# Kernel optimization log

Measured on AMD Instinct MI355X. Metric: run time of the kernel, lower is better.

Reference implementation:

```python
import jax, jax.numpy as jnp
import numpy as np

HIDDEN = 1024
HEADS = 16
HEAD_DIM = HIDDEN // HEADS


def setup_inputs() -> dict:
    key = jax.random.key(0)
    ks = jax.random.split(key, 5)
    B, T = 4, 2048
    x = jax.random.normal(ks[0], (B, T, HIDDEN), dtype=jnp.float32)
    s = 1.0 / np.sqrt(HIDDEN)
    qkv_w = jax.random.normal(ks[1], (HIDDEN, 3 * HIDDEN), dtype=jnp.float32) * s
    qkv_b = jnp.zeros((3 * HIDDEN,), dtype=jnp.float32)
    proj_w = jax.random.normal(ks[2], (HIDDEN, HIDDEN), dtype=jnp.float32) * s
    proj_b = jnp.zeros((HIDDEN,), dtype=jnp.float32)
    return {"x": x, "qkv_w": qkv_w, "qkv_b": qkv_b, "proj_w": proj_w, "proj_b": proj_b}


def reference(x, qkv_w, qkv_b, proj_w, proj_b):
    B, T, C = x.shape
    qkv = x @ qkv_w + qkv_b                       # [B,T,3C]
    qkv = qkv.reshape(B, T, 3, HEADS, HEAD_DIM)
    q, k, v = qkv[:, :, 0], qkv[:, :, 1], qkv[:, :, 2]  # [B,T,H,D]
    scale = HEAD_DIM ** -0.5
    scores = jnp.einsum('bthd,bshd->bhts', q, k) * scale  # [B,H,T,T]
    attn = jax.nn.softmax(scores, axis=-1)
    out = jnp.einsum('bhts,bshd->bthd', attn, v).reshape(B, T, C)
    return out @ proj_w + proj_b
```

## Files before the change

kernel.cpp:

```cpp
#include <hip/hip_runtime.h>
#include <hip/hip_bf16.h>

#define HID  1024
#define N3   3072
#define NH   16
#define HD   64
#define SEQ  2048
#define NB   4
#define MTOT 8192

typedef unsigned short u16x8 __attribute__((ext_vector_type(8)));
typedef unsigned short u16x4 __attribute__((ext_vector_type(4)));
typedef float f32x4 __attribute__((ext_vector_type(4)));

static __device__ __forceinline__ unsigned short f2bf(float f) {
    union { float f; unsigned u; } v; v.f = f;
    unsigned r = (v.u + 0x7fffu + ((v.u >> 16) & 1u)) >> 16;
    return (unsigned short)r;
}

static __device__ __forceinline__ float fexp2(float x) {
    float r; asm("v_exp_f32 %0, %1" : "=v"(r) : "v"(x)); return r;
}

typedef __attribute__((address_space(3))) void* lds_vp;
typedef const __attribute__((address_space(1))) void* gbl_vp;

static __device__ __forceinline__ void gload16(const void* g, void* l) {
    __builtin_amdgcn_global_load_lds((gbl_vp)g, (lds_vp)l, 16, 0, 0);
}

#define CQ 0.18033688011112042f

__device__ __forceinline__ void tcvt_tile(const float* __restrict__ W,
                                          unsigned short* __restrict__ WT,
                                          int R, int C, int tile, int tid,
                                          unsigned short* tilebuf) {
    int tiles_c = C >> 6;
    int k0 = (tile / tiles_c) << 6;
    int n0 = (tile % tiles_c) << 6;
    #pragma unroll
    for (int it = 0; it < 2; ++it) {
        int task = it * 256 + tid;
        int t = task >> 3, dc = task & 7;
        const float* src = W + (size_t)(k0 + t) * C + n0 + dc * 8;
        float4 a = *(const float4*)src;
        float4 b = *(const float4*)(src + 4);
        u16x8 p;
        p[0]=f2bf(a.x); p[1]=f2bf(a.y); p[2]=f2bf(a.z); p[3]=f2bf(a.w);
        p[4]=f2bf(b.x); p[5]=f2bf(b.y); p[6]=f2bf(b.z); p[7]=f2bf(b.w);
        *(u16x8*)&tilebuf[t * 64 + ((dc ^ (t & 7)) << 3)] = p;
    }
    __syncthreads();
    #pragma unroll
    for (int it = 0; it < 2; ++it) {
        int task = it * 256 + tid;
        int d = task >> 3, tc = task & 7;
        u16x8 p;
        #pragma unroll
        for (int i = 0; i < 8; ++i) {
            int ii = (i + tc) & 7;
            int t = tc * 8 + ii;
            p[ii] = tilebuf[t * 64 + ((((d >> 3) ^ (t & 7)) << 3)) + (d & 7)];
        }
        *(u16x8*)(WT + (size_t)(n0 + d) * R + k0 + tc * 8) = p;
    }
}

__global__ __launch_bounds__(256) void k_prep(const float* __restrict__ x,
                                              unsigned short* __restrict__ xb,
                                              const float* __restrict__ qkv_w,
                                              unsigned short* __restrict__ wqkvT,
                                              const float* __restrict__ proj_w,
                                              unsigned short* __restrict__ wprojT) {
    __shared__ unsigned short tilebuf[64 * 64];
    int blk = blockIdx.x, tid = threadIdx.x;
    if (blk < 4096) {
        int i = (blk * 256 + tid) * 8;
        float4 a = *(const float4*)(x + i);
        float4 b = *(const float4*)(x + i + 4);
        u16x8 p;
        p[0]=f2bf(a.x); p[1]=f2bf(a.y); p[2]=f2bf(a.z); p[3]=f2bf(a.w);
        p[4]=f2bf(b.x); p[5]=f2bf(b.y); p[6]=f2bf(b.z); p[7]=f2bf(b.w);
        *(u16x8*)(xb + i) = p;
    } else if (blk < 4864) {
        tcvt_tile(qkv_w, wqkvT, HID, N3, blk - 4096, tid, tilebuf);
    } else {
        tcvt_tile(proj_w, wprojT, HID, HID, blk - 4864, tid, tilebuf);
    }
}

template<int MODE>
__global__ __launch_bounds__(256) void k_gemm(const unsigned short* __restrict__ A,
                                              const unsigned short* __restrict__ BT,
                                              const float* __restrict__ bias,
                                              void* __restrict__ C1, void* __restrict__ C2,
                                              int M, int N, int K) {
    int tiles_n = N >> 7;
    int bid = (blockIdx.x & 7) * (gridDim.x >> 3) + (blockIdx.x >> 3);
    int bm = bid / tiles_n, bn = bid % tiles_n;
    int tid = threadIdx.x, wid = tid >> 6, lane = tid & 63;
    int wr = wid >> 1, wc = wid & 1;
    int fr = lane & 15, fg = lane >> 4;

    __shared__ unsigned short lA[128 * 64];
    __shared__ unsigned short lB[128 * 64];

    f32x4 acc[4][4];
    #pragma unroll
    for (int m = 0; m < 4; ++m)
        #pragma unroll
        for (int n = 0; n < 4; ++n)
            acc[m][n] = (f32x4){0.f, 0.f, 0.f, 0.f};

    int srow = lane >> 3;
    int sch  = (lane & 7) ^ srow;
    const unsigned short* aSrc[4]; const unsigned short* bSrc[4];
    unsigned short* aDst[4]; unsigned short* bDst[4];
    #pragma unroll
    for (int i = 0; i < 4; ++i) {
        int rbase = i * 32 + wid * 8;
        aSrc[i] = A  + (size_t)(bm * 128 + rbase + srow) * K + sch * 8;
        bSrc[i] = BT + (size_t)(bn * 128 + rbase + srow) * K + sch * 8;
        aDst[i] = lA + rbase * 64;
        bDst[i] = lB + rbase * 64;
    }

    for (int k0 = 0; k0 < K; k0 += 64) {
        __syncthreads();
        #pragma unroll
        for (int i = 0; i < 4; ++i) {
            gload16(aSrc[i] + k0, aDst[i]);
            gload16(bSrc[i] + k0, bDst[i]);
        }
        asm volatile("s_waitcnt vmcnt(0)" ::: "memory");
        __syncthreads();
        #pragma unroll
        for (int kk = 0; kk < 2; ++kk) {
            u16x8 af[4], bf[4];
            #pragma unroll
            for (int m = 0; m < 4; ++m) {
                int row = wr * 64 + m * 16 + fr;
                int ch = ((kk << 2) + fg) ^ (fr & 7);
                af[m] = *(const u16x8*)&lA[row * 64 + ch * 8];
            }
            #pragma unroll
            for (int n = 0; n < 4; ++n) {
                int row = wc * 64 + n * 16 + fr;
                int ch = ((kk << 2) + fg) ^ (fr & 7);
                bf[n] = *(const u16x8*)&lB[row * 64 + ch * 8];
            }
            #pragma unroll
            for (int m = 0; m < 4; ++m)
                #pragma unroll
                for (int n = 0; n < 4; ++n)
                    acc[m][n] = __builtin_amdgcn_mfma_f32_16x16x32_bf16(af[m], bf[n], acc[m][n], 0, 0, 0);
        }
    }

    if (MODE == 0) {
        float* C = (float*)C1;
        #pragma unroll
        for (int n = 0; n < 4; ++n) {
            int col = bn * 128 + wc * 64 + n * 16 + fr;
            float bv = bias[col];
            #pragma unroll
            for (int m = 0; m < 4; ++m) {
                int row0 = bm * 128 + wr * 64 + m * 16 + fg * 4;
                #pragma unroll
                for (int r = 0; r < 4; ++r)
                    C[(size_t)(row0 + r) * N + col] = acc[m][n][r] + bv;
            }
        }
    } else {
        if (bn < 16) {
            unsigned short* qkb = (unsigned short*)C1;
            #pragma unroll
            for (int n = 0; n < 4; ++n) {
                int col = bn * 128 + wc * 64 + n * 16 + fr;
                float bv = bias[col];
                float cs = (col < 1024) ? CQ : 1.0f;
                #pragma unroll
                for (int m = 0; m < 4; ++m) {
                    int row0 = bm * 128 + wr * 64 + m * 16 + fg * 4;
                    #pragma unroll
                    for (int r = 0; r < 4; ++r)
                        qkb[(size_t)(row0 + r) * 2048 + col] = f2bf((acc[m][n][r] + bv) * cs);
                }
            }
        } else {
            unsigned short* vT = (unsigned short*)C2;
            #pragma unroll
            for (int n = 0; n < 4; ++n) {
                int col = bn * 128 + wc * 64 + n * 16 + fr;
                float bv = bias[col];
                int cv = col - 2048;
                int hh = cv >> 6, d = cv & 63;
                #pragma unroll
                for (int m = 0; m < 4; ++m) {
                    int row0 = bm * 128 + wr * 64 + m * 16 + fg * 4;
                    int bb = row0 >> 11, t0 = row0 & 2047;
                    u16x4 st;
                    #pragma unroll
                    for (int r = 0; r < 4; ++r) st[r] = f2bf(acc[m][n][r] + bv);
                    *(u16x4*)&vT[((size_t)((bb * 16 + hh) * 64 + d)) * 2048 + t0] = st;
                }
            }
        }
    }
}

__global__ __launch_bounds__(256) void k_attn(const unsigned short* __restrict__ qkb,
                                              const unsigned short* __restrict__ vT,
                                              unsigned short* __restrict__ out) {
    int bid = (blockIdx.x & 7) * 128 + (blockIdx.x >> 3);
    int bh = bid >> 4;
    int q0 = (bid & 15) << 7;
    int b = bh >> 4, h = bh & 15;
    int tid = threadIdx.x, wid = tid >> 6, lane = tid & 63;
    int fr = lane & 15, fg = lane >> 4;

    __shared__ unsigned short lK[2][8192];
    __shared__ unsigned short lV[2][8192];
    const char* lKb = (const char*)lK;
    const char* lVb = (const char*)lV;

    int srow = lane >> 3;
    int sch  = (lane & 7) ^ srow;
    int woff = wid * 512;

    u16x8 ones;
    #pragma unroll
    for (int i = 0; i < 8; ++i) ones[i] = 0x3F80;

    int kfb[2], vbb[4];
    #pragma unroll
    for (int kk = 0; kk < 2; ++kk) kfb[kk] = fr * 128 + (((((kk << 2) + fg) ^ (fr & 7))) << 4);
    #pragma unroll
    for (int kk = 0; kk < 4; ++kk) vbb[kk] = fr * 256 + (((((kk << 2) + fg) ^ (fr & 7))) << 4);

    const unsigned short* qbase = qkb + (size_t)(b * SEQ) * 2048 + h * 64;
    #pragma unroll
    for (int i = 0; i < 4; ++i) {
        int rbase = i * 32 + wid * 8;
        gload16(qbase + (size_t)(q0 + rbase + srow) * 2048 + sch * 8, (unsigned short*)lK + rbase * 64);
    }
    asm volatile("s_waitcnt vmcnt(0)" ::: "memory");
    __syncthreads();
    u16x8 qf[2][2];
    #pragma unroll
    for (int j = 0; j < 2; ++j)
        #pragma unroll
        for (int kk = 0; kk < 2; ++kk)
            qf[j][kk] = *(const u16x8*)(lKb + kfb[kk] + (wid * 32 + j * 16) * 128);
    __syncthreads();

    f32x4 o[2][4];
    #pragma unroll
    for (int j = 0; j < 2; ++j)
        #pragma unroll
        for (int i = 0; i < 4; ++i)
            o[j][i] = (f32x4){0.f, 0.f, 0.f, 0.f};
    f32x4 o_sum[2];
    o_sum[0] = (f32x4){0.f, 0.f, 0.f, 0.f};
    o_sum[1] = (f32x4){0.f, 0.f, 0.f, 0.f};

    const unsigned short* kp[4]; const unsigned short* vp[4];
    {
        const unsigned short* kbase = qkb + (size_t)(b * SEQ) * 2048 + 1024 + h * 64;
        const unsigned short* vbase = vT + (size_t)(bh * 64) * SEQ;
        #pragma unroll
        for (int i = 0; i < 4; ++i) {
            kp[i] = kbase + (size_t)(i * 32 + wid * 8 + srow) * 2048 + sch * 8;
            int vrow = i * 16 + wid * 4 + (lane >> 4);
            int vch = (lane & 15) ^ (vrow & 7);
            vp[i] = vbase + (size_t)vrow * SEQ + vch * 8;
        }
    }

#define STAGE(bufi) do {                                                   \
        unsigned short* kd = (unsigned short*)lK + (bufi) * 8192 + woff;   \
        unsigned short* vd = (unsigned short*)lV + (bufi) * 8192 + woff;   \
        _Pragma("unroll")                                                  \
        for (int i = 0; i < 4; ++i) {                                      \
            gload16(kp[i], kd + i * 2048);  kp[i] += 128 * 2048;           \
            gload16(vp[i], vd + i * 2048);  vp[i] += 128;                  \
        }                                                                  \
    } while (0)

    STAGE(0);

    for (int t = 0; t < 16; ++t) {
        int cur = t & 1;
        int cb = cur * 16384;
        if (t < 15) {
            STAGE(cur ^ 1);
            asm volatile("s_waitcnt vmcnt(8)" ::: "memory");
        } else {
            asm volatile("s_waitcnt vmcnt(0)" ::: "memory");
        }
        __builtin_amdgcn_s_barrier();
        __builtin_amdgcn_sched_barrier(0);

        u16x8 pb[2][4];
        #pragma unroll
        for (int ih = 0; ih < 2; ++ih) {
            f32x4 sa[2][4];
            #pragma unroll
            for (int j = 0; j < 2; ++j)
                #pragma unroll
                for (int il = 0; il < 4; ++il)
                    sa[j][il] = (f32x4){0.f, 0.f, 0.f, 0.f};
            #pragma unroll
            for (int kk = 0; kk < 2; ++kk) {
                u16x8 kf[4];
                #pragma unroll
                for (int il = 0; il < 4; ++il)
                    kf[il] = *(const u16x8*)(lKb + cb + kfb[kk] + (ih * 4 + il) * 2048);
                #pragma unroll
                for (int j = 0; j < 2; ++j)
                    #pragma unroll
                    for (int il = 0; il < 4; ++il)
                        sa[j][il] = __builtin_amdgcn_mfma_f32_16x16x32_bf16(kf[il], qf[j][kk], sa[j][il], 0, 0, 0);
            }

            #pragma unroll
            for (int j = 0; j < 2; ++j) {
                unsigned pk[2][2][2];
                #pragma unroll
                for (int il = 0; il < 4; ++il) {
                    #pragma unroll
                    for (int p = 0; p < 2; ++p) {
                        float ea = fexp2(sa[j][il][2 * p]);
                        float eb = fexp2(sa[j][il][2 * p + 1]);
                        unsigned rr;
                        asm("v_cvt_pk_bf16_f32 %0, %1, %2" : "=v"(rr) : "v"(ea), "v"(eb));
                        pk[il >> 1][il & 1][p] = rr;
                    }
                }
                #pragma unroll
                for (int t2 = 0; t2 < 2; ++t2) {
                    #pragma unroll
                    for (int p = 0; p < 2; ++p) {
                        asm("v_permlane32_swap_b32 %0, %1" : "+v"(pk[t2][0][p]), "+v"(pk[t2][1][p]));
                        asm("v_permlane16_swap_b32 %0, %1" : "+v"(pk[t2][0][p]), "+v"(pk[t2][1][p]));
                    }
                    union { unsigned u[4]; u16x8 v; } w;
                    w.u[0] = pk[t2][0][0]; w.u[1] = pk[t2][0][1];
                    w.u[2] = pk[t2][1][0]; w.u[3] = pk[t2][1][1];
                    pb[j][ih * 2 + t2] = w.v;
                    o_sum[j] = __builtin_amdgcn_mfma_f32_16x16x32_bf16(ones, pb[j][ih * 2 + t2], o_sum[j], 0, 0, 0);
                }
            }
        }

        #pragma unroll
        for (int kk = 0; kk < 4; ++kk) {
            u16x8 vb[4];
            #pragma unroll
            for (int i = 0; i < 4; ++i)
                vb[i] = *(const u16x8*)(lVb + cb + vbb[kk] + i * 4096);
            #pragma unroll
            for (int j = 0; j < 2; ++j)
                #pragma unroll
                for (int i = 0; i < 4; ++i)
                    o[j][i] = __builtin_amdgcn_mfma_f32_16x16x32_bf16(vb[i], pb[j][kk], o[j][i], 0, 0, 0);
        }

        __syncthreads();
    }
#undef STAGE

    #pragma unroll
    for (int j = 0; j < 2; ++j) {
        float inv = 1.f / o_sum[j][0];
        size_t t = q0 + wid * 32 + j * 16 + fr;
        #pragma unroll
        for (int i = 0; i < 4; ++i) {
            u16x4 st;
            st[0] = f2bf(o[j][i][0] * inv);
            st[1] = f2bf(o[j][i][1] * inv);
            st[2] = f2bf(o[j][i][2] * inv);
            st[3] = f2bf(o[j][i][3] * inv);
            *(u16x4*)&out[(size_t)(b * SEQ + t) * HID + h * 64 + i * 16 + fg * 4] = st;
        }
    }
}

extern "C" void kernel_launch(void* const* d_in, const int* in_sizes, int n_in,
                              void* d_out, int out_size, void* d_ws, size_t ws_size,
                              hipStream_t stream) {
    const float* x      = (const float*)d_in[0];
    const float* qkv_w  = (const float*)d_in[1];
    const float* qkv_b  = (const float*)d_in[2];
    const float* proj_w = (const float*)d_in[3];
    const float* proj_b = (const float*)d_in[4];
    float* out = (float*)d_out;

    char* ws = (char*)d_ws;
    unsigned short* xb     = (unsigned short*)ws;
    unsigned short* wqkvT  = (unsigned short*)(ws + 16777216);
    unsigned short* wprojT = (unsigned short*)(ws + 23068672);
    unsigned short* qkb    = (unsigned short*)(ws + 25165824);
    unsigned short* vTb    = (unsigned short*)(ws + 58720256);
    unsigned short* aob    = (unsigned short*)(ws + 75497472);

    k_prep<<<5120, 256, 0, stream>>>(x, xb, qkv_w, wqkvT, proj_w, wprojT);
    k_gemm<1><<<1536, 256, 0, stream>>>(xb, wqkvT, qkv_b, (void*)qkb, (void*)vTb, MTOT, N3, HID);
    k_attn<<<1024, 256, 0, stream>>>(qkb, vTb, aob);
    k_gemm<0><<<512, 256, 0, stream>>>(aob, wprojT, proj_b, (void*)out, nullptr, MTOT, HID, HID);
}
```

Before: 199.3 us.

## Double-buffer GEMM LDS stages and enlarge tiles to 256x128 with 512 threads

The GEMM kernel now uses 512-thread blocks computing 256x128 output tiles, with two dynamic-LDS buffers so the global-to-LDS load of the next K tile overlaps MFMA work on the current one. Grids are halved to match the larger tiles. This targets global-load latency stalls and the per-tile barrier cost, and raises reuse of each B tile. In exchange, each block needs 96KB of LDS, which limits occupancy, and the launch now also makes host-side attribute calls.

```diff
diff --git a/kernel.cpp b/kernel.cpp
--- a/kernel.cpp
+++ b/kernel.cpp
@@ -91,20 +91,20 @@
 }
 
 template<int MODE>
-__global__ __launch_bounds__(256) void k_gemm(const unsigned short* __restrict__ A,
-                                              const unsigned short* __restrict__ BT,
-                                              const float* __restrict__ bias,
-                                              void* __restrict__ C1, void* __restrict__ C2,
-                                              int M, int N, int K) {
+__global__ __launch_bounds__(512, 2) void k_gemm(const unsigned short* __restrict__ A,
+                                                 const unsigned short* __restrict__ BT,
+                                                 const float* __restrict__ bias,
+                                                 void* __restrict__ C1, void* __restrict__ C2,
+                                                 int M, int N, int K) {
+    extern __shared__ char ls[];
     int tiles_n = N >> 7;
     int bid = (blockIdx.x & 7) * (gridDim.x >> 3) + (blockIdx.x >> 3);
     int bm = bid / tiles_n, bn = bid % tiles_n;
     int tid = threadIdx.x, wid = tid >> 6, lane = tid & 63;
     int wr = wid >> 1, wc = wid & 1;
     int fr = lane & 15, fg = lane >> 4;
-
-    __shared__ unsigned short lA[128 * 64];
-    __shared__ unsigned short lB[128 * 64];
+    int srow = lane >> 3;
+    int sch  = (lane & 7) ^ srow;
 
     f32x4 acc[4][4];
     #pragma unroll
@@ -113,50 +113,61 @@
         for (int n = 0; n < 4; ++n)
             acc[m][n] = (f32x4){0.f, 0.f, 0.f, 0.f};
 
-    int srow = lane >> 3;
-    int sch  = (lane & 7) ^ srow;
-    const unsigned short* aSrc[4]; const unsigned short* bSrc[4];
-    unsigned short* aDst[4]; unsigned short* bDst[4];
-    #pragma unroll
-    for (int i = 0; i < 4; ++i) {
-        int rbase = i * 32 + wid * 8;
-        aSrc[i] = A  + (size_t)(bm * 128 + rbase + srow) * K + sch * 8;
-        bSrc[i] = BT + (size_t)(bn * 128 + rbase + srow) * K + sch * 8;
-        aDst[i] = lA + rbase * 64;
-        bDst[i] = lB + rbase * 64;
-    }
-
-    for (int k0 = 0; k0 < K; k0 += 64) {
-        __syncthreads();
-        #pragma unroll
-        for (int i = 0; i < 4; ++i) {
-            gload16(aSrc[i] + k0, aDst[i]);
-            gload16(bSrc[i] + k0, bDst[i]);
-        }
-        asm volatile("s_waitcnt vmcnt(0)" ::: "memory");
-        __syncthreads();
+    const unsigned short* aSrc[4]; const unsigned short* bSrc[2];
+    #pragma unroll
+    for (int i = 0; i < 4; ++i)
+        aSrc[i] = A + (size_t)(bm * 256 + wid * 32 + i * 8 + srow) * K + sch * 8;
+    #pragma unroll
+    for (int i = 0; i < 2; ++i)
+        bSrc[i] = BT + (size_t)(bn * 128 + wid * 16 + i * 8 + srow) * K + sch * 8;
+
+#define GSTAGE(bufi, koff) do {                                              \
+        unsigned short* la = (unsigned short*)(ls + (bufi) * 49152);         \
+        unsigned short* lb = (unsigned short*)(ls + (bufi) * 49152 + 32768); \
+        _Pragma("unroll")                                                    \
+        for (int i = 0; i < 4; ++i)                                          \
+            gload16(aSrc[i] + (koff), la + (wid * 32 + i * 8) * 64);         \
+        _Pragma("unroll")                                                    \
+        for (int i = 0; i < 2; ++i)                                          \
+            gload16(bSrc[i] + (koff), lb + (wid * 16 + i * 8) * 64);         \
+    } while (0)
+
+    GSTAGE(0, 0);
+
+    int ntiles = K >> 6;
+    for (int t = 0; t < ntiles; ++t) {
+        int cb = (t & 1) * 49152;
+        if (t < ntiles - 1) {
+            GSTAGE((t + 1) & 1, (t + 1) * 64);
+            asm volatile("s_waitcnt vmcnt(6)" ::: "memory");
+        } else {
+            asm volatile("s_waitcnt vmcnt(0)" ::: "memory");
+        }
+        __builtin_amdgcn_s_barrier();
+        __builtin_amdgcn_sched_barrier(0);
+
+        const char* la = ls + cb;
+        const char* lb = ls + cb + 32768;
         #pragma unroll
         for (int kk = 0; kk < 2; ++kk) {
             u16x8 af[4], bf[4];
-            #pragma unroll
-            for (int m = 0; m < 4; ++m) {
-                int row = wr * 64 + m * 16 + fr;
-                int ch = ((kk << 2) + fg) ^ (fr & 7);
-                af[m] = *(const u16x8*)&lA[row * 64 + ch * 8];
-            }
-            #pragma unroll
-            for (int n = 0; n < 4; ++n) {
-                int row = wc * 64 + n * 16 + fr;
-                int ch = ((kk << 2) + fg) ^ (fr & 7);
-                bf[n] = *(const u16x8*)&lB[row * 64 + ch * 8];
-            }
+            int chb = ((((kk << 2) + fg) ^ (fr & 7))) << 4;
+            #pragma unroll
+            for (int m = 0; m < 4; ++m)
+                af[m] = *(const u16x8*)(la + (wr * 64 + m * 16 + fr) * 128 + chb);
+            #pragma unroll
+            for (int n = 0; n < 4; ++n)
+                bf[n] = *(const u16x8*)(lb + (wc * 64 + n * 16 + fr) * 128 + chb);
             #pragma unroll
             for (int m = 0; m < 4; ++m)
                 #pragma unroll
                 for (int n = 0; n < 4; ++n)
                     acc[m][n] = __builtin_amdgcn_mfma_f32_16x16x32_bf16(af[m], bf[n], acc[m][n], 0, 0, 0);
         }
-    }
+
+        __syncthreads();
+    }
+#undef GSTAGE
 
     if (MODE == 0) {
         float* C = (float*)C1;
@@ -166,7 +177,7 @@
             float bv = bias[col];
             #pragma unroll
             for (int m = 0; m < 4; ++m) {
-                int row0 = bm * 128 + wr * 64 + m * 16 + fg * 4;
+                int row0 = bm * 256 + wr * 64 + m * 16 + fg * 4;
                 #pragma unroll
                 for (int r = 0; r < 4; ++r)
                     C[(size_t)(row0 + r) * N + col] = acc[m][n][r] + bv;
@@ -182,7 +193,7 @@
                 float cs = (col < 1024) ? CQ : 1.0f;
                 #pragma unroll
                 for (int m = 0; m < 4; ++m) {
-                    int row0 = bm * 128 + wr * 64 + m * 16 + fg * 4;
+                    int row0 = bm * 256 + wr * 64 + m * 16 + fg * 4;
                     #pragma unroll
                     for (int r = 0; r < 4; ++r)
                         qkb[(size_t)(row0 + r) * 2048 + col] = f2bf((acc[m][n][r] + bv) * cs);
@@ -198,7 +209,7 @@
                 int hh = cv >> 6, d = cv & 63;
                 #pragma unroll
                 for (int m = 0; m < 4; ++m) {
-                    int row0 = bm * 128 + wr * 64 + m * 16 + fg * 4;
+                    int row0 = bm * 256 + wr * 64 + m * 16 + fg * 4;
                     int bb = row0 >> 11, t0 = row0 & 2047;
                     u16x4 st;
                     #pragma unroll
@@ -405,8 +416,13 @@
     unsigned short* vTb    = (unsigned short*)(ws + 58720256);
     unsigned short* aob    = (unsigned short*)(ws + 75497472);
 
+    hipFuncSetAttribute(reinterpret_cast<const void*>(&k_gemm<1>),
+                        hipFuncAttributeMaxDynamicSharedMemorySize, 98304);
+    hipFuncSetAttribute(reinterpret_cast<const void*>(&k_gemm<0>),
+                        hipFuncAttributeMaxDynamicSharedMemorySize, 98304);
+
     k_prep<<<5120, 256, 0, stream>>>(x, xb, qkv_w, wqkvT, proj_w, wprojT);
-    k_gemm<1><<<1536, 256, 0, stream>>>(xb, wqkvT, qkv_b, (void*)qkb, (void*)vTb, MTOT, N3, HID);
+    k_gemm<1><<<768, 512, 98304, stream>>>(xb, wqkvT, qkv_b, (void*)qkb, (void*)vTb, MTOT, N3, HID);
     k_attn<<<1024, 256, 0, stream>>>(qkb, vTb, aob);
-    k_gemm<0><<<512, 256, 0, stream>>>(aob, wprojT, proj_b, (void*)out, nullptr, MTOT, HID, HID);
-}
+    k_gemm<0><<<256, 512, 98304, stream>>>(aob, wprojT, proj_b, (void*)out, nullptr, MTOT, HID, HID);
+}
```

Result: faster. 191.2 us (median of 2 runs) (-4.1%).
